# Kernel optimization log

Measured on AMD Instinct MI355X. Metric: run time of the kernel, lower is better.

The kernel has to match this reference:

```python
import jax, jax.numpy as jnp
import numpy as np

EMBED = 768
HEADS = 12
FACTOR = 2
LN_EPS = 1e-5


def layer_norm(x, gamma, beta):
    mu = jnp.mean(x, axis=-1, keepdims=True)
    var = jnp.mean(jnp.square(x - mu), axis=-1, keepdims=True)
    return (x - mu) * jax.lax.rsqrt(var + LN_EPS) * gamma + beta


def setup_inputs() -> dict:
    key = jax.random.key(0)
    ks = jax.random.split(key, 8)
    B, S, E = 8, 1024, EMBED
    H = FACTOR * E
    s_e = 1.0 / np.sqrt(E)
    s_h = 1.0 / np.sqrt(H)
    return {
        "x": jax.random.normal(ks[0], (B, S, E), jnp.float32),
        "Wq": jax.random.normal(ks[1], (E, E), jnp.float32) * s_e,
        "Wk": jax.random.normal(ks[2], (E, E), jnp.float32) * s_e,
        "Wv": jax.random.normal(ks[3], (E, E), jnp.float32) * s_e,
        "W1": jax.random.normal(ks[4], (E, H), jnp.float32) * s_e,
        "b1": jnp.zeros((H,), jnp.float32),
        "W2": jax.random.normal(ks[5], (H, E), jnp.float32) * s_h,
        "b2": jnp.zeros((E,), jnp.float32),
        "g1": jnp.ones((E,), jnp.float32),
        "beta1": jnp.zeros((E,), jnp.float32),
        "g2": jnp.ones((E,), jnp.float32),
        "beta2": jnp.zeros((E,), jnp.float32),
    }


def reference(x, Wq, Wk, Wv, W1, b1, W2, b2, g1, beta1, g2, beta2):
    B, S, E = x.shape
    hd = E // HEADS
    # NOTE: original reshapes (B,S,E)->(B,H,S,hd) WITHOUT transposing heads
    # (non-standard: mixes sequence blocks across heads) - replicated faithfully.
    q = (x @ Wq).reshape(B, HEADS, S, hd)
    k = (x @ Wk).reshape(B, HEADS, S, hd)
    v = (x @ Wv).reshape(B, HEADS, S, hd)
    # no 1/sqrt(d) scaling in the original
    attn = jax.nn.softmax(jnp.einsum('bnqd,bnkd->bnqk', q, k), axis=-1)
    # NOTE: original einsum 'bnqk,bnvd->bnqd' sums over BOTH k and v
    # (value is sum-pooled over its sequence axis) - replicated faithfully.
    out = jnp.einsum('bnqk,bnvd->bnqd', attn, v)
    out = out.transpose(0, 2, 1, 3).reshape(B, S, E)
    a = x + layer_norm(out, g1, beta1)
    # GELU after BOTH linears (exact GELU, torch default)
    h = jax.nn.gelu(a @ W1 + b1, approximate=False)
    m = jax.nn.gelu(h @ W2 + b2, approximate=False)
    return x + layer_norm(m, g2, beta2)
```

## Files before the change

kernel.cpp:

```cpp
#include <hip/hip_runtime.h>
#include <hip/hip_bf16.h>
#include <math.h>

#define E_ 768
#define HID_ 1536
#define SQ_ 1024

typedef unsigned short u16;
using bf16x8 = __attribute__((ext_vector_type(8))) __bf16;
using f32x4  = __attribute__((ext_vector_type(4))) float;

__device__ __forceinline__ u16 f2bf(float f) {
  union { float f; unsigned u; } v; v.f = f;
  unsigned r = v.u + 0x7FFFu + ((v.u >> 16) & 1u);
  return (u16)(r >> 16);
}
__device__ __forceinline__ float bf2f(u16 h) {
  union { unsigned u; float f; } v; v.u = ((unsigned)h) << 16; return v.f;
}
__device__ __forceinline__ float gelu_f(float x) {
  return 0.5f * x * (1.0f + erff(x * 0.70710678118654752f));
}

#define GLDS16(gp, sp) __builtin_amdgcn_global_load_lds( \
    (__attribute__((address_space(1))) const void*)(const void*)(gp), \
    (__attribute__((address_space(3))) void*)(void*)(sp), 16, 0, 0)

__global__ void prep_kernel(const float* __restrict__ x, const float* __restrict__ W1,
                            const float* __restrict__ W2, u16* __restrict__ xb,
                            u16* __restrict__ W1T, u16* __restrict__ W2T) {
  __shared__ float T[64 * 65];
  int bid = blockIdx.x, t = threadIdx.x;
  if (bid < 6144) {
    int base = bid * 1024 + t * 4;
    const float4 v = *reinterpret_cast<const float4*>(x + base);
    ushort4 o; o.x = f2bf(v.x); o.y = f2bf(v.y); o.z = f2bf(v.z); o.w = f2bf(v.w);
    *reinterpret_cast<ushort4*>(xb + base) = o;
    return;
  }
  const float* in; u16* out; int R_in, C_in, rt, ct;
  if (bid < 6432) {
    int b2 = bid - 6144; in = W1; out = W1T; R_in = 768; C_in = 1536;
    rt = b2 / 24; ct = b2 % 24;
  } else {
    int b3 = bid - 6432; in = W2; out = W2T; R_in = 1536; C_in = 768;
    rt = b3 / 12; ct = b3 % 12;
  }
  int r0 = rt << 6, c0 = ct << 6;
  int tr = t >> 4, tc4 = (t & 15) << 2;
#pragma unroll
  for (int i = 0; i < 4; ++i) {
    int row = tr + (i << 4);
    const float4 v = *reinterpret_cast<const float4*>(in + (size_t)(r0 + row) * C_in + c0 + tc4);
    T[row * 65 + tc4 + 0] = v.x;
    T[row * 65 + tc4 + 1] = v.y;
    T[row * 65 + tc4 + 2] = v.z;
    T[row * 65 + tc4 + 3] = v.w;
  }
  __syncthreads();
#pragma unroll
  for (int i = 0; i < 4; ++i) {
    int orow = tr + (i << 4);
    ushort4 o;
    o.x = f2bf(T[(tc4 + 0) * 65 + orow]);
    o.y = f2bf(T[(tc4 + 1) * 65 + orow]);
    o.z = f2bf(T[(tc4 + 2) * 65 + orow]);
    o.w = f2bf(T[(tc4 + 3) * 65 + orow]);
    *reinterpret_cast<ushort4*>(out + (size_t)(c0 + orow) * R_in + r0 + tc4) = o;
  }
}

__global__ void rowsum_kernel(const u16* __restrict__ xb, float* __restrict__ Rp) {
  int bid = blockIdx.x;
  int r = bid >> 2, c = bid & 3;
  int b = r / 12, n = r % 12;
  int t = threadIdx.x;
  int u0 = n << 10;
  int s_lo = u0 / 12;
  int s_hi = (u0 + 1023) / 12;
  int cnt = s_hi - s_lo + 1;
  int cs = s_lo + (cnt * c) / 4;
  int ce = s_lo + (cnt * (c + 1)) / 4;
  float acc[12][3];
#pragma unroll
  for (int g = 0; g < 12; ++g)
    for (int q = 0; q < 3; ++q) acc[g][q] = 0.f;
  const u16* xp = xb + (size_t)b * SQ_ * E_;
  for (int s = cs; s < ce; ++s) {
    float v0 = bf2f(xp[(size_t)s * E_ + t]);
    float v1 = bf2f(xp[(size_t)s * E_ + t + 256]);
    float v2 = bf2f(xp[(size_t)s * E_ + t + 512]);
    int du = 12 * s - u0;
#pragma unroll
    for (int g = 0; g < 12; ++g) {
      int u = du + g;
      if (u >= 0 && u < 1024) { acc[g][0] += v0; acc[g][1] += v1; acc[g][2] += v2; }
    }
  }
  float* Rr = Rp + (size_t)bid * 9216;
#pragma unroll
  for (int g = 0; g < 12; ++g) {
    Rr[g * 768 + t]       = acc[g][0];
    Rr[g * 768 + t + 256] = acc[g][1];
    Rr[g * 768 + t + 512] = acc[g][2];
  }
}

__global__ void ygemm_kernel(const float* __restrict__ Rp, const float* __restrict__ Wv,
                             float* __restrict__ P3) {
  int g = blockIdx.x, r = blockIdx.y, jc = blockIdx.z;
  int t = threadIdx.x;
  int d = t & 63, sub = t >> 6;
  const float* R0 = Rp + (size_t)r * 4 * 9216 + g * 768;
  const float* wp = Wv + g * 64 + d;
  int j0 = jc * 96 + sub * 24;
  float a0 = 0.f, a1 = 0.f, a2 = 0.f, a3 = 0.f;
#pragma unroll
  for (int jj = 0; jj < 24; jj += 4) {
    int j = j0 + jj;
    float r0v = R0[j + 0] + R0[9216 + j + 0] + R0[18432 + j + 0] + R0[27648 + j + 0];
    float r1v = R0[j + 1] + R0[9216 + j + 1] + R0[18432 + j + 1] + R0[27648 + j + 1];
    float r2v = R0[j + 2] + R0[9216 + j + 2] + R0[18432 + j + 2] + R0[27648 + j + 2];
    float r3v = R0[j + 3] + R0[9216 + j + 3] + R0[18432 + j + 3] + R0[27648 + j + 3];
    a0 += r0v * wp[(size_t)(j + 0) * 768];
    a1 += r1v * wp[(size_t)(j + 1) * 768];
    a2 += r2v * wp[(size_t)(j + 2) * 768];
    a3 += r3v * wp[(size_t)(j + 3) * 768];
  }
  __shared__ float red[256];
  red[t] = (a0 + a1) + (a2 + a3);
  __syncthreads();
  if (sub == 0)
    P3[(((size_t)r * 12 + g) * 8 + jc) * 64 + d] = red[d] + red[64 + d] + red[128 + d] + red[192 + d];
}

__global__ void ysum_kernel(const float* __restrict__ P3, float* __restrict__ Y) {
  int bn = blockIdx.x;
  int t = threadIdx.x;
  int d = t & 63, sub = t >> 6;
  const float* Pp = P3 + (size_t)bn * 6144 + d;
  int g0 = sub * 24;
  float s = 0.f;
#pragma unroll 8
  for (int gj = 0; gj < 24; ++gj) s += Pp[(g0 + gj) << 6];
  __shared__ float red[256];
  red[t] = s;
  __syncthreads();
  if (sub == 0)
    Y[bn * 64 + d] = red[d] + red[64 + d] + red[128 + d] + red[192 + d];
}

__global__ void ln1_kernel(const float* __restrict__ Y, const float* __restrict__ g1,
                           const float* __restrict__ be1, float* __restrict__ L1) {
  int b = blockIdx.x, t = threadIdx.x;
  float y0 = Y[b * 768 + t];
  float y1 = Y[b * 768 + t + 256];
  float y2 = Y[b * 768 + t + 512];
  float s = y0 + y1 + y2;
  float sq = y0 * y0 + y1 * y1 + y2 * y2;
  __shared__ float red[8];
#pragma unroll
  for (int o = 32; o > 0; o >>= 1) { s += __shfl_down(s, o, 64); sq += __shfl_down(sq, o, 64); }
  if ((t & 63) == 0) { red[(t >> 6) * 2] = s; red[(t >> 6) * 2 + 1] = sq; }
  __syncthreads();
  s  = red[0] + red[2] + red[4] + red[6];
  sq = red[1] + red[3] + red[5] + red[7];
  float mu = s * (1.f / 768.f);
  float var = sq * (1.f / 768.f) - mu * mu;
  float rs = rsqrtf(var + 1e-5f);
  L1[b * 768 + t]       = (y0 - mu) * rs * g1[t]       + be1[t];
  L1[b * 768 + t + 256] = (y1 - mu) * rs * g1[t + 256] + be1[t + 256];
  L1[b * 768 + t + 512] = (y2 - mu) * rs * g1[t + 512] + be1[t + 512];
}

__global__ void c1_kernel(const float* __restrict__ L1, const float* __restrict__ W1,
                          const float* __restrict__ b1, float* __restrict__ C1) {
  int bid = blockIdx.x;
  int b = bid / 48, c = bid % 48;
  int t = threadIdx.x;
  __shared__ float Ls[768];
  __shared__ float red[8][32];
  for (int q = t; q < 768; q += 256) Ls[q] = L1[b * 768 + q];
  __syncthreads();
  int tc = t & 31, ts = t >> 5;
  int n = c * 32 + tc;
  float acc = 0.f;
  int j0 = ts * 96;
#pragma unroll 4
  for (int j = j0; j < j0 + 96; ++j) acc += Ls[j] * W1[(size_t)j * HID_ + n];
  red[ts][tc] = acc;
  __syncthreads();
  if (ts == 0) {
    float s = b1[n];
#pragma unroll
    for (int k = 0; k < 8; ++k) s += red[k][tc];
    C1[b * HID_ + n] = s;
  }
}

template <int MODE>
__global__ __launch_bounds__(256, 2) void gemm_bt_kernel(
    const u16* __restrict__ A, const u16* __restrict__ BT,
    const float* __restrict__ bias, void* __restrict__ out0, void* __restrict__ out1,
    int N, int lda, int ldb) {
  __shared__ __align__(16) u16 As[128 * 64];
  __shared__ __align__(16) u16 Bs[128 * 64];
  int bid = blockIdx.x;
  int xcd = bid & 7, idx = bid >> 3;
  int mloc, n_, k_off, kk = 0;
  if (MODE == 0) { mloc = idx / 12; n_ = idx % 12; k_off = 0; }
  else           { kk = idx / 48; int rem = idx % 48; mloc = rem / 6; n_ = rem % 6; k_off = kk * 768; }
  int bm = (xcd * 8 + mloc) << 7, bn = n_ << 7;

  int t = threadIdx.x;
  int lane = t & 63, w = t >> 6;
  int wm = (w >> 1) << 6, wn = (w & 1) << 6;
  int quad = lane >> 4, l16 = lane & 15;
  f32x4 acc[4][4] = {};

  for (int k0 = 0; k0 < 768; k0 += 64) {
    __syncthreads();
#pragma unroll
    for (int i = 0; i < 4; ++i) {
      int ci = t + (i << 8);
      int r = ci >> 3, csw = ci & 7;
      int kc = csw ^ (r & 7);
      const u16* ga = A + (size_t)(bm + r) * lda + k_off + k0 + (kc << 3);
      GLDS16(ga, As + ci * 8);
      const u16* gb = BT + (size_t)(bn + r) * ldb + k_off + k0 + (kc << 3);
      GLDS16(gb, Bs + ci * 8);
    }
    __builtin_amdgcn_s_waitcnt(0);
    __syncthreads();
#pragma unroll
    for (int ks = 0; ks < 2; ++ks) {
      bf16x8 af[4], bf[4];
      int kc = (ks << 2) + quad;
#pragma unroll
      for (int mt = 0; mt < 4; ++mt) {
        int row = wm + (mt << 4) + l16;
        af[mt] = *reinterpret_cast<const bf16x8*>(As + row * 64 + ((kc ^ (row & 7)) << 3));
      }
#pragma unroll
      for (int nt = 0; nt < 4; ++nt) {
        int row = wn + (nt << 4) + l16;
        bf[nt] = *reinterpret_cast<const bf16x8*>(Bs + row * 64 + ((kc ^ (row & 7)) << 3));
      }
#pragma unroll
      for (int mt = 0; mt < 4; ++mt)
#pragma unroll
        for (int nt = 0; nt < 4; ++nt)
          acc[mt][nt] = __builtin_amdgcn_mfma_f32_16x16x32_bf16(af[mt], bf[nt], acc[mt][nt], 0, 0, 0);
    }
  }

#pragma unroll
  for (int mt = 0; mt < 4; ++mt) {
    int row0 = bm + wm + (mt << 4) + (quad << 2);
#pragma unroll
    for (int nt = 0; nt < 4; ++nt) {
      int col = bn + wn + (nt << 4) + l16;
      float bv = (MODE == 0) ? bias[(bm >> 10) * N + col] : 0.f;
#pragma unroll
      for (int rr = 0; rr < 4; ++rr) {
        float v = acc[mt][nt][rr] + bv;
        size_t idxo = (size_t)(row0 + rr) * N + col;
        if (MODE == 0)       ((u16*)out0)[idxo] = f2bf(gelu_f(v));
        else if (kk == 0)    ((u16*)out0)[idxo] = f2bf(v);
        else                 ((u16*)out1)[idxo] = f2bf(v);
      }
    }
  }
}

__global__ void ln2_kernel(const u16* __restrict__ p0, const u16* __restrict__ p1,
                           const float* __restrict__ x, const float* __restrict__ b2,
                           const float* __restrict__ g2, const float* __restrict__ be2,
                           float* __restrict__ out) {
  int row = blockIdx.x, t = threadIdx.x;
  float v0 = 0.f, v1 = 0.f, v2 = 0.f, v3 = 0.f;
  float s = 0.f, sq = 0.f;
  int e = t << 2;
  if (t < 192) {
    ushort4 pa = *reinterpret_cast<const ushort4*>(p0 + (size_t)row * 768 + e);
    ushort4 pb = *reinterpret_cast<const ushort4*>(p1 + (size_t)row * 768 + e);
    float4 bb = *reinterpret_cast<const float4*>(b2 + e);
    v0 = gelu_f(bf2f(pa.x) + bf2f(pb.x) + bb.x);
    v1 = gelu_f(bf2f(pa.y) + bf2f(pb.y) + bb.y);
    v2 = gelu_f(bf2f(pa.z) + bf2f(pb.z) + bb.z);
    v3 = gelu_f(bf2f(pa.w) + bf2f(pb.w) + bb.w);
    s = (v0 + v1) + (v2 + v3);
    sq = (v0 * v0 + v1 * v1) + (v2 * v2 + v3 * v3);
  }
  __shared__ float red[8];
#pragma unroll
  for (int o = 32; o > 0; o >>= 1) { s += __shfl_down(s, o, 64); sq += __shfl_down(sq, o, 64); }
  if ((t & 63) == 0) { red[(t >> 6) * 2] = s; red[(t >> 6) * 2 + 1] = sq; }
  __syncthreads();
  s  = red[0] + red[2] + red[4];
  sq = red[1] + red[3] + red[5];
  float mu = s * (1.f / 768.f);
  float var = sq * (1.f / 768.f) - mu * mu;
  float rs = rsqrtf(var + 1e-5f);
  if (t < 192) {
    float4 gg = *reinterpret_cast<const float4*>(g2 + e);
    float4 be = *reinterpret_cast<const float4*>(be2 + e);
    float4 xx = *reinterpret_cast<const float4*>(x + (size_t)row * 768 + e);
    float4 o;
    o.x = xx.x + (v0 - mu) * rs * gg.x + be.x;
    o.y = xx.y + (v1 - mu) * rs * gg.y + be.y;
    o.z = xx.z + (v2 - mu) * rs * gg.z + be.z;
    o.w = xx.w + (v3 - mu) * rs * gg.w + be.w;
    *reinterpret_cast<float4*>(out + (size_t)row * 768 + e) = o;
  }
}

extern "C" void kernel_launch(void* const* d_in, const int* in_sizes, int n_in,
                              void* d_out, int out_size, void* d_ws, size_t ws_size,
                              hipStream_t stream) {
  const float* x   = (const float*)d_in[0];
  const float* Wv  = (const float*)d_in[3];
  const float* W1  = (const float*)d_in[4];
  const float* b1  = (const float*)d_in[5];
  const float* W2  = (const float*)d_in[6];
  const float* b2  = (const float*)d_in[7];
  const float* g1  = (const float*)d_in[8];
  const float* be1 = (const float*)d_in[9];
  const float* g2  = (const float*)d_in[10];
  const float* be2 = (const float*)d_in[11];
  float* out = (float*)d_out;

  char* ws = (char*)d_ws;
  u16*   xb  = (u16*)(ws);
  u16*   W1T = (u16*)(ws + 12582912);
  u16*   W2T = (u16*)(ws + 14942208);
  u16*   h   = (u16*)(ws + 17301504);
  float* Rp  = (float*)(ws + 17301504);
  float* P3  = (float*)(ws + 42467328);
  float* Y   = (float*)(ws + 44826624);
  float* L1  = (float*)(ws + 44851200);
  float* C1  = (float*)(ws + 44875776);
  u16*   m0  = (u16*)(ws + 44924928);
  u16*   p1  = xb;

  prep_kernel<<<6720, 256, 0, stream>>>(x, W1, W2, xb, W1T, W2T);
  rowsum_kernel<<<384, 256, 0, stream>>>(xb, Rp);
  ygemm_kernel<<<dim3(12, 96, 8), 256, 0, stream>>>(Rp, Wv, P3);
  ysum_kernel<<<96, 256, 0, stream>>>(P3, Y);
  ln1_kernel<<<8, 256, 0, stream>>>(Y, g1, be1, L1);
  c1_kernel<<<384, 256, 0, stream>>>(L1, W1, b1, C1);
  gemm_bt_kernel<0><<<768, 256, 0, stream>>>(xb, W1T, C1, (void*)h, nullptr, 1536, 768, 768);
  gemm_bt_kernel<1><<<768, 256, 0, stream>>>(h, W2T, nullptr, (void*)m0, (void*)p1, 768, 1536, 1536);
  ln2_kernel<<<8192, 256, 0, stream>>>(m0, p1, x, b2, g2, be2, out);
}
```

Baseline: 237.1 us.

## Double-buffer 256x256 GEMM tiles with 8 waves and fuse LN1 into c1

The bf16 GEMM moves from 128x128 tiles with 4 waves and a single LDS buffer to 256x256 tiles with 8 waves. It double-buffers the LDS so the next K-slice's global-to-LDS loads run during the MFMAs, and splits each step into quadrants with barriers and setprio to interleave LDS reads with MFMA. The separate LN1 kernel is folded into c1_kernel, which saves one launch and the L1 round trip. The grid shrinks to 192 blocks, so fewer CUs are occupied on a 256-CU part, and the larger accumulator set raises register pressure.

```diff
diff --git a/kernel.cpp b/kernel.cpp
--- a/kernel.cpp
+++ b/kernel.cpp
@@ -150,37 +150,32 @@
     Y[bn * 64 + d] = red[d] + red[64 + d] + red[128 + d] + red[192 + d];
 }
 
-__global__ void ln1_kernel(const float* __restrict__ Y, const float* __restrict__ g1,
-                           const float* __restrict__ be1, float* __restrict__ L1) {
-  int b = blockIdx.x, t = threadIdx.x;
-  float y0 = Y[b * 768 + t];
-  float y1 = Y[b * 768 + t + 256];
-  float y2 = Y[b * 768 + t + 512];
-  float s = y0 + y1 + y2;
-  float sq = y0 * y0 + y1 * y1 + y2 * y2;
-  __shared__ float red[8];
-#pragma unroll
-  for (int o = 32; o > 0; o >>= 1) { s += __shfl_down(s, o, 64); sq += __shfl_down(sq, o, 64); }
-  if ((t & 63) == 0) { red[(t >> 6) * 2] = s; red[(t >> 6) * 2 + 1] = sq; }
-  __syncthreads();
-  s  = red[0] + red[2] + red[4] + red[6];
-  sq = red[1] + red[3] + red[5] + red[7];
-  float mu = s * (1.f / 768.f);
-  float var = sq * (1.f / 768.f) - mu * mu;
-  float rs = rsqrtf(var + 1e-5f);
-  L1[b * 768 + t]       = (y0 - mu) * rs * g1[t]       + be1[t];
-  L1[b * 768 + t + 256] = (y1 - mu) * rs * g1[t + 256] + be1[t + 256];
-  L1[b * 768 + t + 512] = (y2 - mu) * rs * g1[t + 512] + be1[t + 512];
-}
-
-__global__ void c1_kernel(const float* __restrict__ L1, const float* __restrict__ W1,
+__global__ void c1_kernel(const float* __restrict__ Y, const float* __restrict__ g1,
+                          const float* __restrict__ be1, const float* __restrict__ W1,
                           const float* __restrict__ b1, float* __restrict__ C1) {
   int bid = blockIdx.x;
   int b = bid / 48, c = bid % 48;
   int t = threadIdx.x;
   __shared__ float Ls[768];
   __shared__ float red[8][32];
-  for (int q = t; q < 768; q += 256) Ls[q] = L1[b * 768 + q];
+  __shared__ float red2[8];
+  float y0 = Y[b * 768 + t];
+  float y1 = Y[b * 768 + t + 256];
+  float y2 = Y[b * 768 + t + 512];
+  float s = y0 + y1 + y2;
+  float sq = y0 * y0 + y1 * y1 + y2 * y2;
+#pragma unroll
+  for (int o = 32; o > 0; o >>= 1) { s += __shfl_down(s, o, 64); sq += __shfl_down(sq, o, 64); }
+  if ((t & 63) == 0) { red2[(t >> 6) * 2] = s; red2[(t >> 6) * 2 + 1] = sq; }
+  __syncthreads();
+  s  = red2[0] + red2[2] + red2[4] + red2[6];
+  sq = red2[1] + red2[3] + red2[5] + red2[7];
+  float mu = s * (1.f / 768.f);
+  float var = sq * (1.f / 768.f) - mu * mu;
+  float rsv = rsqrtf(var + 1e-5f);
+  Ls[t]       = (y0 - mu) * rsv * g1[t]       + be1[t];
+  Ls[t + 256] = (y1 - mu) * rsv * g1[t + 256] + be1[t + 256];
+  Ls[t + 512] = (y2 - mu) * rsv * g1[t + 512] + be1[t + 512];
   __syncthreads();
   int tc = t & 31, ts = t >> 5;
   int n = c * 32 + tc;
@@ -191,71 +186,136 @@
   red[ts][tc] = acc;
   __syncthreads();
   if (ts == 0) {
-    float s = b1[n];
-#pragma unroll
-    for (int k = 0; k < 8; ++k) s += red[k][tc];
-    C1[b * HID_ + n] = s;
+    float sv = b1[n];
+#pragma unroll
+    for (int k = 0; k < 8; ++k) sv += red[k][tc];
+    C1[b * HID_ + n] = sv;
   }
 }
 
 template <int MODE>
-__global__ __launch_bounds__(256, 2) void gemm_bt_kernel(
+__global__ __launch_bounds__(512, 2) void gemm_bt_kernel(
     const u16* __restrict__ A, const u16* __restrict__ BT,
     const float* __restrict__ bias, void* __restrict__ out0, void* __restrict__ out1,
     int N, int lda, int ldb) {
-  __shared__ __align__(16) u16 As[128 * 64];
-  __shared__ __align__(16) u16 Bs[128 * 64];
+  __shared__ __align__(16) u16 As[2][256 * 64];
+  __shared__ __align__(16) u16 Bs[2][256 * 64];
   int bid = blockIdx.x;
   int xcd = bid & 7, idx = bid >> 3;
   int mloc, n_, k_off, kk = 0;
-  if (MODE == 0) { mloc = idx / 12; n_ = idx % 12; k_off = 0; }
-  else           { kk = idx / 48; int rem = idx % 48; mloc = rem / 6; n_ = rem % 6; k_off = kk * 768; }
-  int bm = (xcd * 8 + mloc) << 7, bn = n_ << 7;
+  if (MODE == 0) { mloc = idx / 6; n_ = idx % 6; k_off = 0; }
+  else           { kk = idx / 12; int rem = idx % 12; mloc = rem / 3; n_ = rem % 3; k_off = kk * 768; }
+  int bm = (xcd * 4 + mloc) << 8, bn = n_ << 8;
 
   int t = threadIdx.x;
   int lane = t & 63, w = t >> 6;
-  int wm = (w >> 1) << 6, wn = (w & 1) << 6;
+  int wm = (w >> 2) << 7, wn = (w & 3) << 6;
   int quad = lane >> 4, l16 = lane & 15;
-  f32x4 acc[4][4] = {};
-
-  for (int k0 = 0; k0 < 768; k0 += 64) {
+  int rx = l16 & 7;
+  f32x4 acc[8][4] = {};
+
+  const u16* Ab = A + (size_t)bm * lda + k_off;
+  const u16* Bb = BT + (size_t)bn * ldb + k_off;
+
+  auto STAGE = [&](int buf, int k0) {
+#pragma unroll
+    for (int i = 0; i < 4; ++i) {
+      int ci = t + (i << 9);
+      int r = ci >> 3;
+      int kc = (ci & 7) ^ (r & 7);
+      GLDS16(Ab + (size_t)r * lda + k0 + (kc << 3), &As[buf][ci << 3]);
+      GLDS16(Bb + (size_t)r * ldb + k0 + (kc << 3), &Bs[buf][ci << 3]);
+    }
+  };
+
+  STAGE(0, 0);
+  __syncthreads();
+
+  bf16x8 af[4][2], bf[4][2];
+#pragma unroll 2
+  for (int tt = 0; tt < 12; ++tt) {
+    int buf = tt & 1;
+    const u16* as = As[buf];
+    const u16* bs = Bs[buf];
+#pragma unroll
+    for (int mt = 0; mt < 4; ++mt) {
+      int ro = (wm + (mt << 4) + l16) * 64;
+#pragma unroll
+      for (int ks = 0; ks < 2; ++ks)
+        af[mt][ks] = *reinterpret_cast<const bf16x8*>(as + ro + ((((ks << 2) + quad) ^ rx) << 3));
+    }
+#pragma unroll
+    for (int nt = 0; nt < 2; ++nt) {
+      int ro = (wn + (nt << 4) + l16) * 64;
+#pragma unroll
+      for (int ks = 0; ks < 2; ++ks)
+        bf[nt][ks] = *reinterpret_cast<const bf16x8*>(bs + ro + ((((ks << 2) + quad) ^ rx) << 3));
+    }
+    if (tt < 11) STAGE(buf ^ 1, (tt + 1) << 6);
+    __builtin_amdgcn_s_barrier();
+    asm volatile("s_waitcnt lgkmcnt(0)" ::: "memory");
+    __builtin_amdgcn_s_setprio(1);
+#pragma unroll
+    for (int mt = 0; mt < 4; ++mt)
+#pragma unroll
+      for (int nt = 0; nt < 2; ++nt)
+#pragma unroll
+        for (int ks = 0; ks < 2; ++ks)
+          acc[mt][nt] = __builtin_amdgcn_mfma_f32_16x16x32_bf16(af[mt][ks], bf[nt][ks], acc[mt][nt], 0, 0, 0);
+    __builtin_amdgcn_s_setprio(0);
+    __builtin_amdgcn_s_barrier();
+#pragma unroll
+    for (int nt = 2; nt < 4; ++nt) {
+      int ro = (wn + (nt << 4) + l16) * 64;
+#pragma unroll
+      for (int ks = 0; ks < 2; ++ks)
+        bf[nt][ks] = *reinterpret_cast<const bf16x8*>(bs + ro + ((((ks << 2) + quad) ^ rx) << 3));
+    }
+    __builtin_amdgcn_s_barrier();
+    asm volatile("s_waitcnt lgkmcnt(0)" ::: "memory");
+    __builtin_amdgcn_s_setprio(1);
+#pragma unroll
+    for (int mt = 0; mt < 4; ++mt)
+#pragma unroll
+      for (int nt = 2; nt < 4; ++nt)
+#pragma unroll
+        for (int ks = 0; ks < 2; ++ks)
+          acc[mt][nt] = __builtin_amdgcn_mfma_f32_16x16x32_bf16(af[mt][ks], bf[nt][ks], acc[mt][nt], 0, 0, 0);
+    __builtin_amdgcn_s_setprio(0);
+    __builtin_amdgcn_s_barrier();
+#pragma unroll
+    for (int mt = 0; mt < 4; ++mt) {
+      int ro = (wm + ((mt + 4) << 4) + l16) * 64;
+#pragma unroll
+      for (int ks = 0; ks < 2; ++ks)
+        af[mt][ks] = *reinterpret_cast<const bf16x8*>(as + ro + ((((ks << 2) + quad) ^ rx) << 3));
+    }
+    __builtin_amdgcn_s_barrier();
+    asm volatile("s_waitcnt lgkmcnt(0)" ::: "memory");
+    __builtin_amdgcn_s_setprio(1);
+#pragma unroll
+    for (int mt = 0; mt < 4; ++mt)
+#pragma unroll
+      for (int nt = 2; nt < 4; ++nt)
+#pragma unroll
+        for (int ks = 0; ks < 2; ++ks)
+          acc[mt + 4][nt] = __builtin_amdgcn_mfma_f32_16x16x32_bf16(af[mt][ks], bf[nt][ks], acc[mt + 4][nt], 0, 0, 0);
+    __builtin_amdgcn_s_setprio(0);
+    __builtin_amdgcn_s_barrier();
+    __builtin_amdgcn_s_setprio(1);
+#pragma unroll
+    for (int mt = 0; mt < 4; ++mt)
+#pragma unroll
+      for (int nt = 0; nt < 2; ++nt)
+#pragma unroll
+        for (int ks = 0; ks < 2; ++ks)
+          acc[mt + 4][nt] = __builtin_amdgcn_mfma_f32_16x16x32_bf16(af[mt][ks], bf[nt][ks], acc[mt + 4][nt], 0, 0, 0);
+    __builtin_amdgcn_s_setprio(0);
     __syncthreads();
-#pragma unroll
-    for (int i = 0; i < 4; ++i) {
-      int ci = t + (i << 8);
-      int r = ci >> 3, csw = ci & 7;
-      int kc = csw ^ (r & 7);
-      const u16* ga = A + (size_t)(bm + r) * lda + k_off + k0 + (kc << 3);
-      GLDS16(ga, As + ci * 8);
-      const u16* gb = BT + (size_t)(bn + r) * ldb + k_off + k0 + (kc << 3);
-      GLDS16(gb, Bs + ci * 8);
-    }
-    __builtin_amdgcn_s_waitcnt(0);
-    __syncthreads();
-#pragma unroll
-    for (int ks = 0; ks < 2; ++ks) {
-      bf16x8 af[4], bf[4];
-      int kc = (ks << 2) + quad;
-#pragma unroll
-      for (int mt = 0; mt < 4; ++mt) {
-        int row = wm + (mt << 4) + l16;
-        af[mt] = *reinterpret_cast<const bf16x8*>(As + row * 64 + ((kc ^ (row & 7)) << 3));
-      }
-#pragma unroll
-      for (int nt = 0; nt < 4; ++nt) {
-        int row = wn + (nt << 4) + l16;
-        bf[nt] = *reinterpret_cast<const bf16x8*>(Bs + row * 64 + ((kc ^ (row & 7)) << 3));
-      }
-#pragma unroll
-      for (int mt = 0; mt < 4; ++mt)
-#pragma unroll
-        for (int nt = 0; nt < 4; ++nt)
-          acc[mt][nt] = __builtin_amdgcn_mfma_f32_16x16x32_bf16(af[mt], bf[nt], acc[mt][nt], 0, 0, 0);
-    }
-  }
-
-#pragma unroll
-  for (int mt = 0; mt < 4; ++mt) {
+  }
+
+#pragma unroll
+  for (int mt = 0; mt < 8; ++mt) {
     int row0 = bm + wm + (mt << 4) + (quad << 2);
 #pragma unroll
     for (int nt = 0; nt < 4; ++nt) {
@@ -338,7 +398,6 @@
   float* Rp  = (float*)(ws + 17301504);
   float* P3  = (float*)(ws + 42467328);
   float* Y   = (float*)(ws + 44826624);
-  float* L1  = (float*)(ws + 44851200);
   float* C1  = (float*)(ws + 44875776);
   u16*   m0  = (u16*)(ws + 44924928);
   u16*   p1  = xb;
@@ -347,9 +406,8 @@
   rowsum_kernel<<<384, 256, 0, stream>>>(xb, Rp);
   ygemm_kernel<<<dim3(12, 96, 8), 256, 0, stream>>>(Rp, Wv, P3);
   ysum_kernel<<<96, 256, 0, stream>>>(P3, Y);
-  ln1_kernel<<<8, 256, 0, stream>>>(Y, g1, be1, L1);
-  c1_kernel<<<384, 256, 0, stream>>>(L1, W1, b1, C1);
-  gemm_bt_kernel<0><<<768, 256, 0, stream>>>(xb, W1T, C1, (void*)h, nullptr, 1536, 768, 768);
-  gemm_bt_kernel<1><<<768, 256, 0, stream>>>(h, W2T, nullptr, (void*)m0, (void*)p1, 768, 1536, 1536);
+  c1_kernel<<<384, 256, 0, stream>>>(Y, g1, be1, W1, b1, C1);
+  gemm_bt_kernel<0><<<192, 512, 0, stream>>>(xb, W1T, C1, (void*)h, nullptr, 1536, 768, 768);
+  gemm_bt_kernel<1><<<192, 512, 0, stream>>>(h, W2T, nullptr, (void*)m0, (void*)p1, 768, 1536, 1536);
   ln2_kernel<<<8192, 256, 0, stream>>>(m0, p1, x, b2, g2, be2, out);
 }
```

New measurement: 249.8 us. 5.3% more time.

## Double-buffer GEMM LDS tiles and fuse LN1 into the c1 kernel

Applied to the files above, without the earlier changes.

The bf16 MFMA GEMM kernel now uses two LDS buffers for A and B. It issues the async global-to-LDS loads for the next k-tile before computing on the current one, so load latency overlaps with MFMA work instead of being serialized by a full waitcnt each iteration. The separate ln1 kernel is folded into c1_kernel: each block recomputes the layer-norm stats of its batch row directly into shared memory, removing one launch and the L1 buffer round trip. The cost is doubled LDS per block, which may limit occupancy, and redundant LN recomputation across the 48 blocks per batch.

```diff
diff --git a/kernel.cpp b/kernel.cpp
--- a/kernel.cpp
+++ b/kernel.cpp
@@ -150,37 +150,32 @@
     Y[bn * 64 + d] = red[d] + red[64 + d] + red[128 + d] + red[192 + d];
 }
 
-__global__ void ln1_kernel(const float* __restrict__ Y, const float* __restrict__ g1,
-                           const float* __restrict__ be1, float* __restrict__ L1) {
-  int b = blockIdx.x, t = threadIdx.x;
+__global__ void c1_kernel(const float* __restrict__ Y, const float* __restrict__ g1,
+                          const float* __restrict__ be1, const float* __restrict__ W1,
+                          const float* __restrict__ b1, float* __restrict__ C1) {
+  int bid = blockIdx.x;
+  int b = bid / 48, c = bid % 48;
+  int t = threadIdx.x;
+  __shared__ float Ls[768];
+  __shared__ float red[8][32];
+  __shared__ float red2[8];
   float y0 = Y[b * 768 + t];
   float y1 = Y[b * 768 + t + 256];
   float y2 = Y[b * 768 + t + 512];
   float s = y0 + y1 + y2;
   float sq = y0 * y0 + y1 * y1 + y2 * y2;
-  __shared__ float red[8];
 #pragma unroll
   for (int o = 32; o > 0; o >>= 1) { s += __shfl_down(s, o, 64); sq += __shfl_down(sq, o, 64); }
-  if ((t & 63) == 0) { red[(t >> 6) * 2] = s; red[(t >> 6) * 2 + 1] = sq; }
-  __syncthreads();
-  s  = red[0] + red[2] + red[4] + red[6];
-  sq = red[1] + red[3] + red[5] + red[7];
+  if ((t & 63) == 0) { red2[(t >> 6) * 2] = s; red2[(t >> 6) * 2 + 1] = sq; }
+  __syncthreads();
+  s  = red2[0] + red2[2] + red2[4] + red2[6];
+  sq = red2[1] + red2[3] + red2[5] + red2[7];
   float mu = s * (1.f / 768.f);
   float var = sq * (1.f / 768.f) - mu * mu;
-  float rs = rsqrtf(var + 1e-5f);
-  L1[b * 768 + t]       = (y0 - mu) * rs * g1[t]       + be1[t];
-  L1[b * 768 + t + 256] = (y1 - mu) * rs * g1[t + 256] + be1[t + 256];
-  L1[b * 768 + t + 512] = (y2 - mu) * rs * g1[t + 512] + be1[t + 512];
-}
-
-__global__ void c1_kernel(const float* __restrict__ L1, const float* __restrict__ W1,
-                          const float* __restrict__ b1, float* __restrict__ C1) {
-  int bid = blockIdx.x;
-  int b = bid / 48, c = bid % 48;
-  int t = threadIdx.x;
-  __shared__ float Ls[768];
-  __shared__ float red[8][32];
-  for (int q = t; q < 768; q += 256) Ls[q] = L1[b * 768 + q];
+  float rsv = rsqrtf(var + 1e-5f);
+  Ls[t]       = (y0 - mu) * rsv * g1[t]       + be1[t];
+  Ls[t + 256] = (y1 - mu) * rsv * g1[t + 256] + be1[t + 256];
+  Ls[t + 512] = (y2 - mu) * rsv * g1[t + 512] + be1[t + 512];
   __syncthreads();
   int tc = t & 31, ts = t >> 5;
   int n = c * 32 + tc;
@@ -191,10 +186,10 @@
   red[ts][tc] = acc;
   __syncthreads();
   if (ts == 0) {
-    float s = b1[n];
-#pragma unroll
-    for (int k = 0; k < 8; ++k) s += red[k][tc];
-    C1[b * HID_ + n] = s;
+    float sv = b1[n];
+#pragma unroll
+    for (int k = 0; k < 8; ++k) sv += red[k][tc];
+    C1[b * HID_ + n] = sv;
   }
 }
 
@@ -203,8 +198,8 @@
     const u16* __restrict__ A, const u16* __restrict__ BT,
     const float* __restrict__ bias, void* __restrict__ out0, void* __restrict__ out1,
     int N, int lda, int ldb) {
-  __shared__ __align__(16) u16 As[128 * 64];
-  __shared__ __align__(16) u16 Bs[128 * 64];
+  __shared__ __align__(16) u16 As[2][128 * 64];
+  __shared__ __align__(16) u16 Bs[2][128 * 64];
   int bid = blockIdx.x;
   int xcd = bid & 7, idx = bid >> 3;
   int mloc, n_, k_off, kk = 0;
@@ -218,20 +213,29 @@
   int quad = lane >> 4, l16 = lane & 15;
   f32x4 acc[4][4] = {};
 
-  for (int k0 = 0; k0 < 768; k0 += 64) {
-    __syncthreads();
+  const u16* Ab = A + (size_t)bm * lda + k_off;
+  const u16* Bb = BT + (size_t)bn * ldb + k_off;
+
+  auto STAGE = [&](int buf, int k0) {
 #pragma unroll
     for (int i = 0; i < 4; ++i) {
       int ci = t + (i << 8);
       int r = ci >> 3, csw = ci & 7;
       int kc = csw ^ (r & 7);
-      const u16* ga = A + (size_t)(bm + r) * lda + k_off + k0 + (kc << 3);
-      GLDS16(ga, As + ci * 8);
-      const u16* gb = BT + (size_t)(bn + r) * ldb + k_off + k0 + (kc << 3);
-      GLDS16(gb, Bs + ci * 8);
+      GLDS16(Ab + (size_t)r * lda + k0 + (kc << 3), &As[buf][ci << 3]);
+      GLDS16(Bb + (size_t)r * ldb + k0 + (kc << 3), &Bs[buf][ci << 3]);
     }
-    __builtin_amdgcn_s_waitcnt(0);
-    __syncthreads();
+  };
+
+  STAGE(0, 0);
+  __syncthreads();
+
+#pragma unroll 2
+  for (int tt = 0; tt < 12; ++tt) {
+    int buf = tt & 1;
+    if (tt < 11) STAGE(buf ^ 1, (tt + 1) << 6);
+    const u16* as = As[buf];
+    const u16* bs = Bs[buf];
 #pragma unroll
     for (int ks = 0; ks < 2; ++ks) {
       bf16x8 af[4], bf[4];
@@ -239,12 +243,12 @@
 #pragma unroll
       for (int mt = 0; mt < 4; ++mt) {
         int row = wm + (mt << 4) + l16;
-        af[mt] = *reinterpret_cast<const bf16x8*>(As + row * 64 + ((kc ^ (row & 7)) << 3));
+        af[mt] = *reinterpret_cast<const bf16x8*>(as + row * 64 + ((kc ^ (row & 7)) << 3));
       }
 #pragma unroll
       for (int nt = 0; nt < 4; ++nt) {
         int row = wn + (nt << 4) + l16;
-        bf[nt] = *reinterpret_cast<const bf16x8*>(Bs + row * 64 + ((kc ^ (row & 7)) << 3));
+        bf[nt] = *reinterpret_cast<const bf16x8*>(bs + row * 64 + ((kc ^ (row & 7)) << 3));
       }
 #pragma unroll
       for (int mt = 0; mt < 4; ++mt)
@@ -252,6 +256,7 @@
         for (int nt = 0; nt < 4; ++nt)
           acc[mt][nt] = __builtin_amdgcn_mfma_f32_16x16x32_bf16(af[mt], bf[nt], acc[mt][nt], 0, 0, 0);
     }
+    __syncthreads();
   }
 
 #pragma unroll
@@ -338,7 +343,6 @@
   float* Rp  = (float*)(ws + 17301504);
   float* P3  = (float*)(ws + 42467328);
   float* Y   = (float*)(ws + 44826624);
-  float* L1  = (float*)(ws + 44851200);
   float* C1  = (float*)(ws + 44875776);
   u16*   m0  = (u16*)(ws + 44924928);
   u16*   p1  = xb;
@@ -347,8 +351,7 @@
   rowsum_kernel<<<384, 256, 0, stream>>>(xb, Rp);
   ygemm_kernel<<<dim3(12, 96, 8), 256, 0, stream>>>(Rp, Wv, P3);
   ysum_kernel<<<96, 256, 0, stream>>>(P3, Y);
-  ln1_kernel<<<8, 256, 0, stream>>>(Y, g1, be1, L1);
-  c1_kernel<<<384, 256, 0, stream>>>(L1, W1, b1, C1);
+  c1_kernel<<<384, 256, 0, stream>>>(Y, g1, be1, W1, b1, C1);
   gemm_bt_kernel<0><<<768, 256, 0, stream>>>(xb, W1T, C1, (void*)h, nullptr, 1536, 768, 768);
   gemm_bt_kernel<1><<<768, 256, 0, stream>>>(h, W2T, nullptr, (void*)m0, (void*)p1, 768, 1536, 1536);
   ln2_kernel<<<8192, 256, 0, stream>>>(m0, p1, x, b2, g2, be2, out);
```

Result: slower. 251.1 us (+5.9%).

## Fuse rowsum, ygemm, ysum, LN1 and C1 into one cooperative kernel

Applied to the files above, without the earlier changes.

Replaces five small sequential launches (rowsum, ygemm, ysum, ln1, c1) with a single cooperative kernel of 384 blocks that uses grid-wide syncs between phases. The ygemm work is spread across the 384 blocks with a loop over 24 virtual blocks, and LN1 is recomputed per block into shared memory, so the L1 buffer is no longer needed. The aim is to remove kernel launch gaps and tail effects for these tiny stages. In exchange it adds grid-sync overhead and may lose some parallelism in the ygemm phase, which previously ran as 9216 blocks.

```diff
diff --git a/kernel.cpp b/kernel.cpp
--- a/kernel.cpp
+++ b/kernel.cpp
@@ -1,6 +1,9 @@
 #include <hip/hip_runtime.h>
 #include <hip/hip_bf16.h>
+#include <hip/hip_cooperative_groups.h>
 #include <math.h>
+
+namespace cg = cooperative_groups;
 
 #define E_ 768
 #define HID_ 1536
@@ -70,131 +73,137 @@
   }
 }
 
-__global__ void rowsum_kernel(const u16* __restrict__ xb, float* __restrict__ Rp) {
+__global__ __launch_bounds__(256, 2) void mid_kernel(
+    const u16* __restrict__ xb, const float* __restrict__ Wv,
+    const float* __restrict__ g1, const float* __restrict__ be1,
+    const float* __restrict__ W1, const float* __restrict__ b1,
+    float* __restrict__ Rp, float* __restrict__ P3,
+    float* __restrict__ Y, float* __restrict__ C1) {
+  cg::grid_group gridg = cg::this_grid();
   int bid = blockIdx.x;
-  int r = bid >> 2, c = bid & 3;
-  int b = r / 12, n = r % 12;
   int t = threadIdx.x;
-  int u0 = n << 10;
-  int s_lo = u0 / 12;
-  int s_hi = (u0 + 1023) / 12;
-  int cnt = s_hi - s_lo + 1;
-  int cs = s_lo + (cnt * c) / 4;
-  int ce = s_lo + (cnt * (c + 1)) / 4;
-  float acc[12][3];
-#pragma unroll
-  for (int g = 0; g < 12; ++g)
-    for (int q = 0; q < 3; ++q) acc[g][q] = 0.f;
-  const u16* xp = xb + (size_t)b * SQ_ * E_;
-  for (int s = cs; s < ce; ++s) {
-    float v0 = bf2f(xp[(size_t)s * E_ + t]);
-    float v1 = bf2f(xp[(size_t)s * E_ + t + 256]);
-    float v2 = bf2f(xp[(size_t)s * E_ + t + 512]);
-    int du = 12 * s - u0;
+  __shared__ float redA[256];
+  __shared__ float Ls[768];
+  __shared__ float redB[8][32];
+  __shared__ float red2[8];
+
+  {
+    int r = bid >> 2, c = bid & 3;
+    int b = r / 12, n = r % 12;
+    int u0 = n << 10;
+    int s_lo = u0 / 12;
+    int s_hi = (u0 + 1023) / 12;
+    int cnt = s_hi - s_lo + 1;
+    int cs = s_lo + (cnt * c) / 4;
+    int ce = s_lo + (cnt * (c + 1)) / 4;
+    float acc[12][3];
+#pragma unroll
+    for (int g = 0; g < 12; ++g)
+      for (int q = 0; q < 3; ++q) acc[g][q] = 0.f;
+    const u16* xp = xb + (size_t)b * SQ_ * E_;
+    for (int s = cs; s < ce; ++s) {
+      float v0 = bf2f(xp[(size_t)s * E_ + t]);
+      float v1 = bf2f(xp[(size_t)s * E_ + t + 256]);
+      float v2 = bf2f(xp[(size_t)s * E_ + t + 512]);
+      int du = 12 * s - u0;
+#pragma unroll
+      for (int g = 0; g < 12; ++g) {
+        int u = du + g;
+        if (u >= 0 && u < 1024) { acc[g][0] += v0; acc[g][1] += v1; acc[g][2] += v2; }
+      }
+    }
+    float* Rr = Rp + (size_t)bid * 9216;
 #pragma unroll
     for (int g = 0; g < 12; ++g) {
-      int u = du + g;
-      if (u >= 0 && u < 1024) { acc[g][0] += v0; acc[g][1] += v1; acc[g][2] += v2; }
-    }
-  }
-  float* Rr = Rp + (size_t)bid * 9216;
-#pragma unroll
-  for (int g = 0; g < 12; ++g) {
-    Rr[g * 768 + t]       = acc[g][0];
-    Rr[g * 768 + t + 256] = acc[g][1];
-    Rr[g * 768 + t + 512] = acc[g][2];
-  }
-}
-
-__global__ void ygemm_kernel(const float* __restrict__ Rp, const float* __restrict__ Wv,
-                             float* __restrict__ P3) {
-  int g = blockIdx.x, r = blockIdx.y, jc = blockIdx.z;
-  int t = threadIdx.x;
-  int d = t & 63, sub = t >> 6;
-  const float* R0 = Rp + (size_t)r * 4 * 9216 + g * 768;
-  const float* wp = Wv + g * 64 + d;
-  int j0 = jc * 96 + sub * 24;
-  float a0 = 0.f, a1 = 0.f, a2 = 0.f, a3 = 0.f;
-#pragma unroll
-  for (int jj = 0; jj < 24; jj += 4) {
-    int j = j0 + jj;
-    float r0v = R0[j + 0] + R0[9216 + j + 0] + R0[18432 + j + 0] + R0[27648 + j + 0];
-    float r1v = R0[j + 1] + R0[9216 + j + 1] + R0[18432 + j + 1] + R0[27648 + j + 1];
-    float r2v = R0[j + 2] + R0[9216 + j + 2] + R0[18432 + j + 2] + R0[27648 + j + 2];
-    float r3v = R0[j + 3] + R0[9216 + j + 3] + R0[18432 + j + 3] + R0[27648 + j + 3];
-    a0 += r0v * wp[(size_t)(j + 0) * 768];
-    a1 += r1v * wp[(size_t)(j + 1) * 768];
-    a2 += r2v * wp[(size_t)(j + 2) * 768];
-    a3 += r3v * wp[(size_t)(j + 3) * 768];
-  }
-  __shared__ float red[256];
-  red[t] = (a0 + a1) + (a2 + a3);
-  __syncthreads();
-  if (sub == 0)
-    P3[(((size_t)r * 12 + g) * 8 + jc) * 64 + d] = red[d] + red[64 + d] + red[128 + d] + red[192 + d];
-}
-
-__global__ void ysum_kernel(const float* __restrict__ P3, float* __restrict__ Y) {
-  int bn = blockIdx.x;
-  int t = threadIdx.x;
-  int d = t & 63, sub = t >> 6;
-  const float* Pp = P3 + (size_t)bn * 6144 + d;
-  int g0 = sub * 24;
-  float s = 0.f;
+      Rr[g * 768 + t]       = acc[g][0];
+      Rr[g * 768 + t + 256] = acc[g][1];
+      Rr[g * 768 + t + 512] = acc[g][2];
+    }
+  }
+  gridg.sync();
+
+  {
+    int d = t & 63, sub = t >> 6;
+    for (int it = 0; it < 24; ++it) {
+      int vb = bid + it * 384;
+      int g = vb % 12;
+      int rem = vb / 12;
+      int r = rem % 96, jc = rem / 96;
+      const float* R0 = Rp + (size_t)r * 4 * 9216 + g * 768;
+      const float* wp = Wv + g * 64 + d;
+      int j0 = jc * 96 + sub * 24;
+      float a0 = 0.f, a1 = 0.f, a2 = 0.f, a3 = 0.f;
+#pragma unroll
+      for (int jj = 0; jj < 24; jj += 4) {
+        int j = j0 + jj;
+        float r0v = R0[j + 0] + R0[9216 + j + 0] + R0[18432 + j + 0] + R0[27648 + j + 0];
+        float r1v = R0[j + 1] + R0[9216 + j + 1] + R0[18432 + j + 1] + R0[27648 + j + 1];
+        float r2v = R0[j + 2] + R0[9216 + j + 2] + R0[18432 + j + 2] + R0[27648 + j + 2];
+        float r3v = R0[j + 3] + R0[9216 + j + 3] + R0[18432 + j + 3] + R0[27648 + j + 3];
+        a0 += r0v * wp[(size_t)(j + 0) * 768];
+        a1 += r1v * wp[(size_t)(j + 1) * 768];
+        a2 += r2v * wp[(size_t)(j + 2) * 768];
+        a3 += r3v * wp[(size_t)(j + 3) * 768];
+      }
+      redA[t] = (a0 + a1) + (a2 + a3);
+      __syncthreads();
+      if (sub == 0)
+        P3[(((size_t)r * 12 + g) * 8 + jc) * 64 + d] =
+            redA[d] + redA[64 + d] + redA[128 + d] + redA[192 + d];
+      __syncthreads();
+    }
+  }
+  gridg.sync();
+
+  if (bid < 96) {
+    int bn = bid;
+    int d = t & 63, sub = t >> 6;
+    const float* Pp = P3 + (size_t)bn * 6144 + d;
+    int g0 = sub * 24;
+    float s = 0.f;
 #pragma unroll 8
-  for (int gj = 0; gj < 24; ++gj) s += Pp[(g0 + gj) << 6];
-  __shared__ float red[256];
-  red[t] = s;
-  __syncthreads();
-  if (sub == 0)
-    Y[bn * 64 + d] = red[d] + red[64 + d] + red[128 + d] + red[192 + d];
-}
-
-__global__ void ln1_kernel(const float* __restrict__ Y, const float* __restrict__ g1,
-                           const float* __restrict__ be1, float* __restrict__ L1) {
-  int b = blockIdx.x, t = threadIdx.x;
-  float y0 = Y[b * 768 + t];
-  float y1 = Y[b * 768 + t + 256];
-  float y2 = Y[b * 768 + t + 512];
-  float s = y0 + y1 + y2;
-  float sq = y0 * y0 + y1 * y1 + y2 * y2;
-  __shared__ float red[8];
-#pragma unroll
-  for (int o = 32; o > 0; o >>= 1) { s += __shfl_down(s, o, 64); sq += __shfl_down(sq, o, 64); }
-  if ((t & 63) == 0) { red[(t >> 6) * 2] = s; red[(t >> 6) * 2 + 1] = sq; }
-  __syncthreads();
-  s  = red[0] + red[2] + red[4] + red[6];
-  sq = red[1] + red[3] + red[5] + red[7];
-  float mu = s * (1.f / 768.f);
-  float var = sq * (1.f / 768.f) - mu * mu;
-  float rs = rsqrtf(var + 1e-5f);
-  L1[b * 768 + t]       = (y0 - mu) * rs * g1[t]       + be1[t];
-  L1[b * 768 + t + 256] = (y1 - mu) * rs * g1[t + 256] + be1[t + 256];
-  L1[b * 768 + t + 512] = (y2 - mu) * rs * g1[t + 512] + be1[t + 512];
-}
-
-__global__ void c1_kernel(const float* __restrict__ L1, const float* __restrict__ W1,
-                          const float* __restrict__ b1, float* __restrict__ C1) {
-  int bid = blockIdx.x;
-  int b = bid / 48, c = bid % 48;
-  int t = threadIdx.x;
-  __shared__ float Ls[768];
-  __shared__ float red[8][32];
-  for (int q = t; q < 768; q += 256) Ls[q] = L1[b * 768 + q];
-  __syncthreads();
-  int tc = t & 31, ts = t >> 5;
-  int n = c * 32 + tc;
-  float acc = 0.f;
-  int j0 = ts * 96;
+    for (int gj = 0; gj < 24; ++gj) s += Pp[(g0 + gj) << 6];
+    redA[t] = s;
+    __syncthreads();
+    if (sub == 0)
+      Y[bn * 64 + d] = redA[d] + redA[64 + d] + redA[128 + d] + redA[192 + d];
+  }
+  gridg.sync();
+
+  {
+    int b = bid / 48, c = bid % 48;
+    float y0 = Y[b * 768 + t];
+    float y1 = Y[b * 768 + t + 256];
+    float y2 = Y[b * 768 + t + 512];
+    float s = y0 + y1 + y2;
+    float sq = y0 * y0 + y1 * y1 + y2 * y2;
+#pragma unroll
+    for (int o = 32; o > 0; o >>= 1) { s += __shfl_down(s, o, 64); sq += __shfl_down(sq, o, 64); }
+    if ((t & 63) == 0) { red2[(t >> 6) * 2] = s; red2[(t >> 6) * 2 + 1] = sq; }
+    __syncthreads();
+    s  = red2[0] + red2[2] + red2[4] + red2[6];
+    sq = red2[1] + red2[3] + red2[5] + red2[7];
+    float mu = s * (1.f / 768.f);
+    float var = sq * (1.f / 768.f) - mu * mu;
+    float rsv = rsqrtf(var + 1e-5f);
+    Ls[t]       = (y0 - mu) * rsv * g1[t]       + be1[t];
+    Ls[t + 256] = (y1 - mu) * rsv * g1[t + 256] + be1[t + 256];
+    Ls[t + 512] = (y2 - mu) * rsv * g1[t + 512] + be1[t + 512];
+    __syncthreads();
+    int tc = t & 31, ts = t >> 5;
+    int n = c * 32 + tc;
+    float acc = 0.f;
+    int j0 = ts * 96;
 #pragma unroll 4
-  for (int j = j0; j < j0 + 96; ++j) acc += Ls[j] * W1[(size_t)j * HID_ + n];
-  red[ts][tc] = acc;
-  __syncthreads();
-  if (ts == 0) {
-    float s = b1[n];
-#pragma unroll
-    for (int k = 0; k < 8; ++k) s += red[k][tc];
-    C1[b * HID_ + n] = s;
+    for (int j = j0; j < j0 + 96; ++j) acc += Ls[j] * W1[(size_t)j * HID_ + n];
+    redB[ts][tc] = acc;
+    __syncthreads();
+    if (ts == 0) {
+      float sv = b1[n];
+#pragma unroll
+      for (int k = 0; k < 8; ++k) sv += redB[k][tc];
+      C1[b * HID_ + n] = sv;
+    }
   }
 }
 
@@ -338,17 +347,19 @@
   float* Rp  = (float*)(ws + 17301504);
   float* P3  = (float*)(ws + 42467328);
   float* Y   = (float*)(ws + 44826624);
-  float* L1  = (float*)(ws + 44851200);
   float* C1  = (float*)(ws + 44875776);
   u16*   m0  = (u16*)(ws + 44924928);
   u16*   p1  = xb;
 
   prep_kernel<<<6720, 256, 0, stream>>>(x, W1, W2, xb, W1T, W2T);
-  rowsum_kernel<<<384, 256, 0, stream>>>(xb, Rp);
-  ygemm_kernel<<<dim3(12, 96, 8), 256, 0, stream>>>(Rp, Wv, P3);
-  ysum_kernel<<<96, 256, 0, stream>>>(P3, Y);
-  ln1_kernel<<<8, 256, 0, stream>>>(Y, g1, be1, L1);
-  c1_kernel<<<384, 256, 0, stream>>>(L1, W1, b1, C1);
+
+  {
+    void* args[] = { (void*)&xb, (void*)&Wv, (void*)&g1, (void*)&be1,
+                     (void*)&W1, (void*)&b1, (void*)&Rp, (void*)&P3,
+                     (void*)&Y, (void*)&C1 };
+    hipLaunchCooperativeKernel((void*)mid_kernel, dim3(384), dim3(256), args, 0, stream);
+  }
+
   gemm_bt_kernel<0><<<768, 256, 0, stream>>>(xb, W1T, C1, (void*)h, nullptr, 1536, 768, 768);
   gemm_bt_kernel<1><<<768, 256, 0, stream>>>(h, W2T, nullptr, (void*)m0, (void*)p1, 768, 1536, 1536);
   ln2_kernel<<<8192, 256, 0, stream>>>(m0, p1, x, b2, g2, be2, out);
```

Result: slower. 394.2 us (+66.2%).
